# Kernel tuning notes

Hardware: AMD Instinct MI355X
Metric: run time of the kernel (lower is better)

## Reference

```python
import jax, jax.numpy as jnp
import numpy as np


def setup_inputs() -> dict:
    key = jax.random.key(0)
    k1, k2, k3, k4 = jax.random.split(key, 4)
    B, M, S, Q = 128, 200, 20, 20
    H, V, D = 3, 50000, 128  # max_hops, num_vocab, embedding_dim
    story = jax.random.randint(k1, (B, M, S), 0, V)
    query = jax.random.randint(k2, (B, Q), 0, V)
    # (max_hops+1) embedding tables, init normal(0, 0.1) as in torch code
    E = jax.random.normal(k3, (H + 1, V, D), dtype=jnp.float32) * 0.1
    # (max_hops+1) temporal encodings [max_story_size, D], normal(0, 0.1)
    T = jax.random.normal(k4, (H + 1, M, D), dtype=jnp.float32) * 0.1
    return {"story": story, "query": query, "E": E, "T": T}


def reference(story, query, E, T):
    max_hops = E.shape[0] - 1
    # u1 = sum over query tokens of B-embedding (hop-0 table)
    u = jnp.sum(E[0][query], axis=1)  # [B, D]
    for hop in range(max_hops):
        # memory: A-embed story, sum over words, add temporal encoding
        m = jnp.sum(E[hop][story], axis=2) + T[hop]        # [B, M, D]
        # attention over memories (legacy F.softmax on 2D -> dim=1)
        uTm = jnp.einsum('bmd,bd->bm', m, u)               # [B, M]
        proba = jax.nn.softmax(uTm, axis=1)
        # output memory representation
        c = jnp.sum(E[hop + 1][story], axis=2) + T[hop + 1]  # [B, M, D]
        o = jnp.einsum('bm,bmd->bd', proba, c)             # [B, D]
        u = u + o
    ahat = u @ E[-1].T  # [B, V]
    return ahat, jax.nn.softmax(ahat, axis=1)
```

## Files before the change

### kernel.cpp

```cpp
#include <hip/hip_runtime.h>
#include <float.h>


constexpr int Bn = 128;
constexpr int Mn = 200;
constexpr int Sn = 20;
constexpr int Qn = 20;
constexpr int Hn = 3;
constexpr int Vn = 50000;
constexpr int Dn = 128;
constexpr int CH = 100;

constexpr int GTILE = 128;
constexpr int NT    = (Vn + GTILE - 1) / GTILE;
constexpr int SMCHK = 10;

constexpr int TSTR = 130;

constexpr size_t MSUM_ELEMS = (size_t)(Hn + 1) * Bn * Mn * Dn;
constexpr size_t SMWS_ELEMS = (size_t)NT * Bn * 2;

typedef float f32x4 __attribute__((ext_vector_type(4)));

__global__ __launch_bounds__(256)
void msum_kernel(const int* __restrict__ story, const float* __restrict__ E,
                 const float* __restrict__ T, float* __restrict__ msum) {
    int slot = threadIdx.x >> 5;
    int l    = threadIdx.x & 31;
    int row  = blockIdx.x * 8 + slot;
    int t    = row / (Bn * Mn);
    int rem  = row - t * (Bn * Mn);
    int b    = rem / Mn;
    int m    = rem - b * Mn;

    const int* st = story + (b * Mn + m) * Sn;
    const float4* Tv = (const float4*)(T) + (size_t)(t * Mn + m) * 32;
    const float4* Et = (const float4*)(E) + (size_t)t * Vn * 32;

    int idx[Sn];
    #pragma unroll
    for (int s = 0; s < Sn; ++s) idx[s] = st[s];

    float4 acc = Tv[l];
    #pragma unroll
    for (int s = 0; s < Sn; ++s) {
        float4 e = Et[(size_t)idx[s] * 32 + l];
        acc.x += e.x; acc.y += e.y; acc.z += e.z; acc.w += e.w;
    }
    f32x4 av = {acc.x, acc.y, acc.z, acc.w};
    __builtin_nontemporal_store(av, (f32x4*)msum + (size_t)row * 32 + l);
}

__global__ __launch_bounds__(1024)
void hops_kernel(const int* __restrict__ query, const float* __restrict__ E,
                 const float* __restrict__ msum, float* __restrict__ ufin) {
    __shared__ __align__(16) float tileA[Mn * TSTR];
    __shared__ float u[Dn];
    __shared__ float sc[Mn];
    __shared__ float op[1024];
    __shared__ float red[16];
    __shared__ float bc[2];

    const int b    = blockIdx.x;
    const int tid  = threadIdx.x;
    const int wave = tid >> 6;
    const int lane = tid & 63;
    const int d    = tid & (Dn - 1);
    const int g    = tid >> 7;
    const int dq   = tid >> 8;
    const int mm   = tid & 255;

    {
        const float* src = msum + ((size_t)0 * Bn + b) * (size_t)(Mn * Dn);
        float2 vbuf[13];
        #pragma unroll
        for (int k = 0; k < 13; ++k) {
            int r = wave + 16 * k;
            if (r < Mn)
                vbuf[k] = *(const float2*)(src + (size_t)r * Dn + 2 * lane);
        }
        #pragma unroll
        for (int k = 0; k < 13; ++k) {
            int r = wave + 16 * k;
            if (r < Mn)
                *(float2*)(tileA + r * TSTR + 2 * lane) = vbuf[k];
        }
    }

    if (tid < Dn) {
        float acc = 0.f;
        const int* q = query + b * Qn;
        #pragma unroll
        for (int j = 0; j < Qn; ++j)
            acc += E[(size_t)q[j] * Dn + tid];
        u[tid] = acc;
    }
    __syncthreads();

    for (int hop = 0; hop < Hn; ++hop) {
        float2 vbuf[13];
        {
            const float* src = msum + ((size_t)(hop + 1) * Bn + b) * (size_t)(Mn * Dn);
            #pragma unroll
            for (int k = 0; k < 13; ++k) {
                int r = wave + 16 * k;
                if (r < Mn)
                    vbuf[k] = *(const float2*)(src + (size_t)r * Dn + 2 * lane);
            }
        }

        if (mm < Mn) {
            float p = 0.f;
            #pragma unroll
            for (int i = 0; i < 32; ++i)
                p += tileA[mm * TSTR + dq * 32 + i] * u[dq * 32 + i];
            op[dq * Mn + mm] = p;
        }
        __syncthreads();

        #pragma unroll
        for (int k = 0; k < 13; ++k) {
            int r = wave + 16 * k;
            if (r < Mn)
                *(float2*)(tileA + r * TSTR + 2 * lane) = vbuf[k];
        }

        float v = -FLT_MAX;
        if (tid < Mn)
            v = op[tid] + op[Mn + tid] + op[2 * Mn + tid] + op[3 * Mn + tid];
        float mx = v;
        #pragma unroll
        for (int off = 32; off; off >>= 1) mx = fmaxf(mx, __shfl_down(mx, off, 64));
        if (lane == 0) red[wave] = mx;
        __syncthreads();
        if (tid == 0) {
            float m0 = red[0];
            #pragma unroll
            for (int i = 1; i < 16; ++i) m0 = fmaxf(m0, red[i]);
            bc[0] = m0;
        }
        __syncthreads();
        float rmax = bc[0];
        float e = (tid < Mn) ? __expf(v - rmax) : 0.f;
        float sm = e;
        #pragma unroll
        for (int off = 32; off; off >>= 1) sm += __shfl_down(sm, off, 64);
        if (lane == 0) red[wave] = sm;
        __syncthreads();
        if (tid == 0) {
            float s = 0.f;
            #pragma unroll
            for (int i = 0; i < 16; ++i) s += red[i];
            bc[1] = s;
        }
        __syncthreads();
        float inv = 1.f / bc[1];
        if (tid < Mn) sc[tid] = e * inv;
        __syncthreads();

        float acc = 0.f;
        #pragma unroll
        for (int k = 0; k < 25; ++k) {
            int m = g + 8 * k;
            acc += sc[m] * tileA[m * TSTR + d];
        }
        op[g * Dn + d] = acc;
        __syncthreads();
        if (tid < Dn) {
            float s = 0.f;
            #pragma unroll
            for (int i = 0; i < 8; ++i) s += op[i * Dn + tid];
            u[tid] += s;
        }
        __syncthreads();
    }
    if (tid < Dn) ufin[b * Dn + tid] = u[tid];
}

__global__ __launch_bounds__(1024)
void hops_fused_kernel(const int* __restrict__ story, const int* __restrict__ query,
                       const float* __restrict__ E, const float* __restrict__ T,
                       float* __restrict__ ufin) {
    __shared__ __align__(16) float tile[CH * Dn];
    __shared__ float u[Dn];
    __shared__ float sc[Mn];
    __shared__ float op[8 * Dn];
    __shared__ float red[16];
    __shared__ float bc[2];

    const int b    = blockIdx.x;
    const int tid  = threadIdx.x;
    const int wave = tid >> 6;
    const int lane = tid & 63;
    const int d    = tid & (Dn - 1);
    const int g    = tid >> 7;
    const int slot = tid >> 5;
    const int l    = tid & 31;
    const int* st  = story + b * (Mn * Sn);

    if (tid < Dn) {
        float acc = 0.f;
        const int* q = query + b * Qn;
        #pragma unroll
        for (int j = 0; j < Qn; ++j)
            acc += E[(size_t)q[j] * Dn + tid];
        u[tid] = acc;
    }

    auto build = [&](int t, int base) {
        const float4* Et = (const float4*)(E) + (size_t)t * Vn * 32;
        const float4* Tt = (const float4*)(T) + (size_t)t * Mn * 32;
        for (int m = base + slot; m < base + CH; m += 32) {
            const int* sm = st + m * Sn;
            float4 acc = Tt[(size_t)m * 32 + l];
            #pragma unroll
            for (int s = 0; s < Sn; ++s) {
                float4 e = Et[(size_t)sm[s] * 32 + l];
                acc.x += e.x; acc.y += e.y; acc.z += e.z; acc.w += e.w;
            }
            ((float4*)tile)[(m - base) * 32 + l] = acc;
        }
    };
    auto scores = [&](int base) {
        for (int m = base + wave; m < base + CH; m += 16) {
            float p = tile[(m - base) * Dn + lane]      * u[lane]
                    + tile[(m - base) * Dn + lane + 64] * u[lane + 64];
            #pragma unroll
            for (int off = 32; off; off >>= 1) p += __shfl_down(p, off, 64);
            if (lane == 0) sc[m] = p;
        }
    };

    for (int hop = 0; hop < Hn; ++hop) {
        if (hop == 0) {
            build(0, 0);  __syncthreads(); scores(0);  __syncthreads();
            build(0, CH); __syncthreads(); scores(CH); __syncthreads();
        } else {
            scores(CH); __syncthreads();
            build(hop, 0); __syncthreads(); scores(0); __syncthreads();
        }

        float v = (tid < Mn) ? sc[tid] : -FLT_MAX;
        float mx = v;
        #pragma unroll
        for (int off = 32; off; off >>= 1) mx = fmaxf(mx, __shfl_down(mx, off, 64));
        if (lane == 0) red[wave] = mx;
        __syncthreads();
        if (tid == 0) {
            float m0 = red[0];
            #pragma unroll
            for (int i = 1; i < 16; ++i) m0 = fmaxf(m0, red[i]);
            bc[0] = m0;
        }
        __syncthreads();
        float rmax = bc[0];
        float e = (tid < Mn) ? __expf(v - rmax) : 0.f;
        float sm = e;
        #pragma unroll
        for (int off = 32; off; off >>= 1) sm += __shfl_down(sm, off, 64);
        if (lane == 0) red[wave] = sm;
        __syncthreads();
        if (tid == 0) {
            float s = 0.f;
            #pragma unroll
            for (int i = 0; i < 16; ++i) s += red[i];
            bc[1] = s;
        }
        __syncthreads();
        float inv = 1.f / bc[1];
        if (tid < Mn) sc[tid] = e * inv;

        float oacc = 0.f;
        build(hop + 1, 0);
        __syncthreads();
        for (int m = g; m < CH; m += 8)
            oacc += sc[m] * tile[m * Dn + d];
        __syncthreads();
        build(hop + 1, CH);
        __syncthreads();
        for (int m = CH + g; m < 2 * CH; m += 8)
            oacc += sc[m] * tile[(m - CH) * Dn + d];
        op[g * Dn + d] = oacc;
        __syncthreads();
        if (tid < Dn) {
            float s = 0.f;
            #pragma unroll
            for (int i = 0; i < 8; ++i) s += op[i * Dn + tid];
            u[tid] += s;
        }
        __syncthreads();
    }

    if (tid < Dn) ufin[b * Dn + tid] = u[tid];
}

constexpr int KC   = 32;
constexpr int LSTR = 140;
__device__ __forceinline__ int ldsCol(int c) { return c + 4 * (c >> 5); }

__global__ __launch_bounds__(256)
void ahat_gemm_kernel(const float* __restrict__ E, const float* __restrict__ ufin,
                      float* __restrict__ out, float* __restrict__ ws2) {
    __shared__ __align__(16) float uA[KC * LSTR];
    __shared__ __align__(16) float eB[KC * LSTR];
    const float* E3 = E + (size_t)Hn * Vn * Dn;

    const int tid   = threadIdx.x;
    const int tr    = tid & 15;
    const int tc    = tid >> 4;
    const int vbase = blockIdx.x * GTILE;

    const int f4 = tid & 7;
    const int rr = tid >> 3;

    float acc[8][8];
    #pragma unroll
    for (int i = 0; i < 8; ++i)
        #pragma unroll
        for (int j = 0; j < 8; ++j) acc[i][j] = 0.f;

    for (int kb = 0; kb < Dn; kb += KC) {
        #pragma unroll
        for (int i = 0; i < 4; ++i) {
            int r   = rr + 32 * i;
            int col = ldsCol(r);
            float4 uv = *(const float4*)(ufin + (size_t)r * Dn + kb + f4 * 4);
            uA[(f4 * 4 + 0) * LSTR + col] = uv.x;
            uA[(f4 * 4 + 1) * LSTR + col] = uv.y;
            uA[(f4 * 4 + 2) * LSTR + col] = uv.z;
            uA[(f4 * 4 + 3) * LSTR + col] = uv.w;
        }
        #pragma unroll
        for (int i = 0; i < 4; ++i) {
            int r  = rr + 32 * i;
            int vg = vbase + r; if (vg > Vn - 1) vg = Vn - 1;
            int col = ldsCol(r);
            float4 ev = *(const float4*)(E3 + (size_t)vg * Dn + kb + f4 * 4);
            eB[(f4 * 4 + 0) * LSTR + col] = ev.x;
            eB[(f4 * 4 + 1) * LSTR + col] = ev.y;
            eB[(f4 * 4 + 2) * LSTR + col] = ev.z;
            eB[(f4 * 4 + 3) * LSTR + col] = ev.w;
        }
        __syncthreads();
        const int ca = ldsCol(tr * 8);
        const int cb = ldsCol(tc * 8);
        #pragma unroll 2
        for (int k = 0; k < KC; ++k) {
            float4 a0 = *(const float4*)&uA[k * LSTR + ca];
            float4 a1 = *(const float4*)&uA[k * LSTR + ca + 4];
            float4 b0 = *(const float4*)&eB[k * LSTR + cb];
            float4 b1 = *(const float4*)&eB[k * LSTR + cb + 4];
            float av[8] = {a0.x, a0.y, a0.z, a0.w, a1.x, a1.y, a1.z, a1.w};
            float bv[8] = {b0.x, b0.y, b0.z, b0.w, b1.x, b1.y, b1.z, b1.w};
            #pragma unroll
            for (int i = 0; i < 8; ++i)
                #pragma unroll
                for (int j = 0; j < 8; ++j)
                    acc[i][j] += av[i] * bv[j];
        }
        __syncthreads();
    }

    const int  v0    = vbase + tc * 8;
    const bool valid = v0 < Vn;
    if (valid) {
        #pragma unroll
        for (int i = 0; i < 8; ++i) {
            int bb = tr * 8 + i;
            *(float4*)(out + (size_t)bb * Vn + v0) =
                make_float4(acc[i][0], acc[i][1], acc[i][2], acc[i][3]);
            *(float4*)(out + (size_t)bb * Vn + v0 + 4) =
                make_float4(acc[i][4], acc[i][5], acc[i][6], acc[i][7]);
        }
    }

    if (ws2) {
        #pragma unroll
        for (int i = 0; i < 8; ++i) {
            float tm = -FLT_MAX, ts = 0.f;
            if (valid) {
                #pragma unroll
                for (int j = 0; j < 8; ++j) tm = fmaxf(tm, acc[i][j]);
                #pragma unroll
                for (int j = 0; j < 8; ++j) ts += __expf(acc[i][j] - tm);
            }
            uA[tc * 128 + tr * 8 + i] = tm;
            eB[tc * 128 + tr * 8 + i] = ts;
        }
        __syncthreads();
        if (tid < Bn) {
            float M = -FLT_MAX;
            #pragma unroll
            for (int t = 0; t < 16; ++t) M = fmaxf(M, uA[t * 128 + tid]);
            float S = 0.f;
            #pragma unroll
            for (int t = 0; t < 16; ++t)
                S += eB[t * 128 + tid] * __expf(uA[t * 128 + tid] - M);
            float2* w = (float2*)ws2;
            w[(size_t)blockIdx.x * Bn + tid] = make_float2(M, S);
        }
    }
}

__global__ __launch_bounds__(256)
void softmax_merge_kernel(const float* __restrict__ ahat, const float* __restrict__ ws2,
                          float* __restrict__ osm) {
    __shared__ float redm[4], reds[4];
    __shared__ float bcM, bcI;

    const int ck   = blockIdx.x;
    const int b    = blockIdx.y;
    const int tid  = threadIdx.x;
    const int wave = tid >> 6;
    const int lane = tid & 63;

    float m = -FLT_MAX, s = 0.f;
    const float2* w = (const float2*)ws2;
    for (int i = tid; i < NT; i += 256) {
        float2 p = w[(size_t)i * Bn + b];
        float nm = fmaxf(m, p.x);
        s = s * __expf(m - nm) + p.y * __expf(p.x - nm);
        m = nm;
    }
    #pragma unroll
    for (int off = 32; off; off >>= 1) {
        float mo = __shfl_down(m, off, 64);
        float so = __shfl_down(s, off, 64);
        float nm = fmaxf(m, mo);
        s = s * __expf(m - nm) + so * __expf(mo - nm);
        m = nm;
    }
    if (lane == 0) { redm[wave] = m; reds[wave] = s; }
    __syncthreads();
    if (tid == 0) {
        float M = redm[0];
        #pragma unroll
        for (int i = 1; i < 4; ++i) M = fmaxf(M, redm[i]);
        float S = 0.f;
        #pragma unroll
        for (int i = 0; i < 4; ++i) S += reds[i] * __expf(redm[i] - M);
        bcM = M; bcI = 1.f / S;
    }
    __syncthreads();
    const float M   = bcM;
    const float inv = bcI;

    constexpr int C4 = Vn / SMCHK / 4;
    const float4* row  = (const float4*)(ahat + (size_t)b * Vn) + (size_t)ck * C4;
    float4*       orow = (float4*)(osm + (size_t)b * Vn) + (size_t)ck * C4;
    for (int v = tid; v < C4; v += 256) {
        float4 x = row[v];
        orow[v] = make_float4(__expf(x.x - M) * inv, __expf(x.y - M) * inv,
                              __expf(x.z - M) * inv, __expf(x.w - M) * inv);
    }
}

__global__ __launch_bounds__(1024)
void softmax_kernel(const float* __restrict__ ahat, float* __restrict__ osm) {
    __shared__ float redm[16];
    __shared__ float reds[16];
    __shared__ float bc2[2];

    int b    = blockIdx.x;
    int tid  = threadIdx.x;
    int wave = tid >> 6;
    int lane = tid & 63;

    const float4* row  = (const float4*)(ahat + (size_t)b * Vn);
    float4*       orow = (float4*)(osm + (size_t)b * Vn);
    constexpr int N4 = Vn / 4;

    float m = -FLT_MAX, s = 0.f;
    for (int v = tid; v < N4; v += 1024) {
        float4 x = row[v];
        float cm = fmaxf(fmaxf(x.x, x.y), fmaxf(x.z, x.w));
        if (cm > m) { s *= __expf(m - cm); m = cm; }
        s += __expf(x.x - m) + __expf(x.y - m) + __expf(x.z - m) + __expf(x.w - m);
    }
    #pragma unroll
    for (int off = 32; off; off >>= 1) {
        float mo = __shfl_down(m, off, 64);
        float so = __shfl_down(s, off, 64);
        float nm = fmaxf(m, mo);
        s = s * __expf(m - nm) + so * __expf(mo - nm);
        m = nm;
    }
    if (lane == 0) { redm[wave] = m; reds[wave] = s; }
    __syncthreads();
    if (tid == 0) {
        float M = redm[0];
        #pragma unroll
        for (int i = 1; i < 16; ++i) M = fmaxf(M, redm[i]);
        float S = 0.f;
        #pragma unroll
        for (int i = 0; i < 16; ++i) S += reds[i] * __expf(redm[i] - M);
        bc2[0] = M; bc2[1] = 1.f / S;
    }
    __syncthreads();
    float rmax = bc2[0];
    float inv  = bc2[1];

    for (int v = tid; v < N4; v += 1024) {
        float4 x = row[v];
        orow[v] = make_float4(__expf(x.x - rmax) * inv, __expf(x.y - rmax) * inv,
                              __expf(x.z - rmax) * inv, __expf(x.w - rmax) * inv);
    }
}

extern "C" void kernel_launch(void* const* d_in, const int* in_sizes, int n_in,
                              void* d_out, int out_size, void* d_ws, size_t ws_size,
                              hipStream_t stream) {
    const int*   story = (const int*)d_in[0];
    const int*   query = (const int*)d_in[1];
    const float* E     = (const float*)d_in[2];
    const float* T     = (const float*)d_in[3];

    float* out  = (float*)d_out;
    float* ufin = out + (size_t)Bn * Vn;

    const bool haveMsum = ws_size >= MSUM_ELEMS * sizeof(float);
    const bool haveSm   = ws_size >= (MSUM_ELEMS + SMWS_ELEMS) * sizeof(float);
    float* msum = (float*)d_ws;
    float* ws2  = haveSm ? ((float*)d_ws + MSUM_ELEMS) : nullptr;

    if (haveMsum) {
        msum_kernel<<<(Hn + 1) * Bn * Mn / 8, 256, 0, stream>>>(story, E, T, msum);
        hops_kernel<<<Bn, 1024, 0, stream>>>(query, E, msum, ufin);
    } else {
        hops_fused_kernel<<<Bn, 1024, 0, stream>>>(story, query, E, T, ufin);
    }

    ahat_gemm_kernel<<<NT, 256, 0, stream>>>(E, ufin, out, ws2);

    if (ws2) {
        softmax_merge_kernel<<<dim3(SMCHK, Bn), 256, 0, stream>>>(
            out, ws2, out + (size_t)Bn * Vn);
    } else {
        softmax_kernel<<<Bn, 1024, 0, stream>>>(out, out + (size_t)Bn * Vn);
    }
}
```

Baseline: 329.3 us.

## Fuse the vocab softmax into the GEMM epilogue via a grid-wide last-block merge

The separate softmax merge kernel is removed. Each GEMM block publishes its per-row partial max and sum and increments an atomic counter. The last block to arrive merges all partials into a global max and inverse sum, then releases a flag. Every block spins on that flag and writes the softmax output directly from its register accumulators, so the logits are no longer re-read from global memory. The msum store also changes from a nontemporal store to a plain store. The spin barrier assumes all 391 blocks are co-resident and adds a grid-wide synchronisation point.

```diff
diff --git a/kernel.cpp b/kernel.cpp
--- a/kernel.cpp
+++ b/kernel.cpp
@@ -13,14 +13,15 @@
 
 constexpr int GTILE = 128;
 constexpr int NT    = (Vn + GTILE - 1) / GTILE;
-constexpr int SMCHK = 10;
 
 constexpr int TSTR = 130;
 
 constexpr size_t MSUM_ELEMS = (size_t)(Hn + 1) * Bn * Mn * Dn;
 constexpr size_t SMWS_ELEMS = (size_t)NT * Bn * 2;
-
-typedef float f32x4 __attribute__((ext_vector_type(4)));
+constexpr size_t SMWS_TOTAL = SMWS_ELEMS + 256 + 8;
+
+#define AT_LD(p)    __hip_atomic_load((p), __ATOMIC_RELAXED, __HIP_MEMORY_SCOPE_AGENT)
+#define AT_ST(p, v) __hip_atomic_store((p), (v), __ATOMIC_RELAXED, __HIP_MEMORY_SCOPE_AGENT)
 
 __global__ __launch_bounds__(256)
 void msum_kernel(const int* __restrict__ story, const float* __restrict__ E,
@@ -47,13 +48,13 @@
         float4 e = Et[(size_t)idx[s] * 32 + l];
         acc.x += e.x; acc.y += e.y; acc.z += e.z; acc.w += e.w;
     }
-    f32x4 av = {acc.x, acc.y, acc.z, acc.w};
-    __builtin_nontemporal_store(av, (f32x4*)msum + (size_t)row * 32 + l);
+    ((float4*)msum)[(size_t)row * 32 + l] = acc;
 }
 
 __global__ __launch_bounds__(1024)
 void hops_kernel(const int* __restrict__ query, const float* __restrict__ E,
-                 const float* __restrict__ msum, float* __restrict__ ufin) {
+                 const float* __restrict__ msum, float* __restrict__ ufin,
+                 unsigned int* __restrict__ ctl) {
     __shared__ __align__(16) float tileA[Mn * TSTR];
     __shared__ float u[Dn];
     __shared__ float sc[Mn];
@@ -69,6 +70,11 @@
     const int g    = tid >> 7;
     const int dq   = tid >> 8;
     const int mm   = tid & 255;
+
+    if (ctl && b == 0 && tid == 0) {
+        AT_ST(ctl + 0, 0u);
+        AT_ST(ctl + 1, 0u);
+    }
 
     {
         const float* src = msum + ((size_t)0 * Bn + b) * (size_t)(Mn * Dn);
@@ -300,9 +306,11 @@
 
 __global__ __launch_bounds__(256)
 void ahat_gemm_kernel(const float* __restrict__ E, const float* __restrict__ ufin,
-                      float* __restrict__ out, float* __restrict__ ws2) {
+                      float* __restrict__ out, float* __restrict__ ws2,
+                      float* __restrict__ osm) {
     __shared__ __align__(16) float uA[KC * LSTR];
     __shared__ __align__(16) float eB[KC * LSTR];
+    __shared__ unsigned int amLast;
     const float* E3 = E + (size_t)Hn * Vn * Dn;
 
     const int tid   = threadIdx.x;
@@ -374,53 +382,129 @@
         }
     }
 
-    if (ws2) {
+    if (!ws2) return;
+
+    float* gs = ws2 + SMWS_ELEMS;
+    unsigned int* ctl = (unsigned int*)(gs + 256);
+
+    #pragma unroll
+    for (int i = 0; i < 8; ++i) {
+        float tm = -FLT_MAX, ts = 0.f;
+        if (valid) {
+            #pragma unroll
+            for (int j = 0; j < 8; ++j) tm = fmaxf(tm, acc[i][j]);
+            #pragma unroll
+            for (int j = 0; j < 8; ++j) ts += __expf(acc[i][j] - tm);
+        }
+        uA[tc * 128 + tr * 8 + i] = tm;
+        eB[tc * 128 + tr * 8 + i] = ts;
+    }
+    __syncthreads();
+    if (tid < Bn) {
+        float M = -FLT_MAX;
+        #pragma unroll
+        for (int t = 0; t < 16; ++t) M = fmaxf(M, uA[t * 128 + tid]);
+        float S = 0.f;
+        #pragma unroll
+        for (int t = 0; t < 16; ++t)
+            S += eB[t * 128 + tid] * __expf(uA[t * 128 + tid] - M);
+        float* wp = ws2 + ((size_t)blockIdx.x * Bn + tid) * 2;
+        AT_ST(wp + 0, M);
+        AT_ST(wp + 1, S);
+    }
+    __syncthreads();
+
+    if (tid == 0) {
+        __threadfence();
+        amLast = (atomicAdd(ctl + 0, 1u) == (unsigned)NT - 1) ? 1u : 0u;
+    }
+    __syncthreads();
+
+    if (amLast) {
+        const int r = tid & 127, h = tid >> 7;
+        float M = -FLT_MAX, S = 0.f;
+        for (int i = h; i < NT; i += 8) {
+            float pm[4], ps[4]; int n = 0;
+            #pragma unroll
+            for (int k = 0; k < 4; ++k) {
+                int t = i + 2 * k;
+                if (t < NT) {
+                    pm[n] = AT_LD(ws2 + ((size_t)t * Bn + r) * 2 + 0);
+                    ps[n] = AT_LD(ws2 + ((size_t)t * Bn + r) * 2 + 1);
+                    ++n;
+                }
+            }
+            for (int k = 0; k < n; ++k) {
+                float nm = fmaxf(M, pm[k]);
+                S = S * __expf(M - nm) + ps[k] * __expf(pm[k] - nm);
+                M = nm;
+            }
+        }
+        uA[h * 128 + r] = M;
+        eB[h * 128 + r] = S;
+        __syncthreads();
+        if (tid < 128) {
+            float m0 = uA[tid], m1 = uA[128 + tid];
+            float s0 = eB[tid], s1 = eB[128 + tid];
+            float nm = fmaxf(m0, m1);
+            float St = s0 * __expf(m0 - nm) + s1 * __expf(m1 - nm);
+            AT_ST(gs + tid * 2 + 0, nm);
+            AT_ST(gs + tid * 2 + 1, 1.f / St);
+        }
+        __syncthreads();
+        if (tid == 0) {
+            __threadfence();
+            __hip_atomic_store(ctl + 1, 1u, __ATOMIC_RELEASE, __HIP_MEMORY_SCOPE_AGENT);
+        }
+    }
+
+    if (tid == 0) {
+        long it = 0;
+        while (__hip_atomic_load(ctl + 1, __ATOMIC_ACQUIRE, __HIP_MEMORY_SCOPE_AGENT) == 0u
+               && it < 100000000L) {
+            ++it;
+            __builtin_amdgcn_s_sleep(8);
+        }
+    }
+    __syncthreads();
+
+    if (valid) {
         #pragma unroll
         for (int i = 0; i < 8; ++i) {
-            float tm = -FLT_MAX, ts = 0.f;
-            if (valid) {
-                #pragma unroll
-                for (int j = 0; j < 8; ++j) tm = fmaxf(tm, acc[i][j]);
-                #pragma unroll
-                for (int j = 0; j < 8; ++j) ts += __expf(acc[i][j] - tm);
-            }
-            uA[tc * 128 + tr * 8 + i] = tm;
-            eB[tc * 128 + tr * 8 + i] = ts;
-        }
-        __syncthreads();
-        if (tid < Bn) {
-            float M = -FLT_MAX;
-            #pragma unroll
-            for (int t = 0; t < 16; ++t) M = fmaxf(M, uA[t * 128 + tid]);
-            float S = 0.f;
-            #pragma unroll
-            for (int t = 0; t < 16; ++t)
-                S += eB[t * 128 + tid] * __expf(uA[t * 128 + tid] - M);
-            float2* w = (float2*)ws2;
-            w[(size_t)blockIdx.x * Bn + tid] = make_float2(M, S);
+            int bb = tr * 8 + i;
+            float M = AT_LD(gs + bb * 2 + 0);
+            float I = AT_LD(gs + bb * 2 + 1);
+            *(float4*)(osm + (size_t)bb * Vn + v0) =
+                make_float4(__expf(acc[i][0] - M) * I, __expf(acc[i][1] - M) * I,
+                            __expf(acc[i][2] - M) * I, __expf(acc[i][3] - M) * I);
+            *(float4*)(osm + (size_t)bb * Vn + v0 + 4) =
+                make_float4(__expf(acc[i][4] - M) * I, __expf(acc[i][5] - M) * I,
+                            __expf(acc[i][6] - M) * I, __expf(acc[i][7] - M) * I);
         }
     }
 }
 
-__global__ __launch_bounds__(256)
-void softmax_merge_kernel(const float* __restrict__ ahat, const float* __restrict__ ws2,
-                          float* __restrict__ osm) {
-    __shared__ float redm[4], reds[4];
-    __shared__ float bcM, bcI;
-
-    const int ck   = blockIdx.x;
-    const int b    = blockIdx.y;
-    const int tid  = threadIdx.x;
-    const int wave = tid >> 6;
-    const int lane = tid & 63;
+__global__ __launch_bounds__(1024)
+void softmax_kernel(const float* __restrict__ ahat, float* __restrict__ osm) {
+    __shared__ float redm[16];
+    __shared__ float reds[16];
+    __shared__ float bc2[2];
+
+    int b    = blockIdx.x;
+    int tid  = threadIdx.x;
+    int wave = tid >> 6;
+    int lane = tid & 63;
+
+    const float4* row  = (const float4*)(ahat + (size_t)b * Vn);
+    float4*       orow = (float4*)(osm + (size_t)b * Vn);
+    constexpr int N4 = Vn / 4;
 
     float m = -FLT_MAX, s = 0.f;
-    const float2* w = (const float2*)ws2;
-    for (int i = tid; i < NT; i += 256) {
-        float2 p = w[(size_t)i * Bn + b];
-        float nm = fmaxf(m, p.x);
-        s = s * __expf(m - nm) + p.y * __expf(p.x - nm);
-        m = nm;
+    for (int v = tid; v < N4; v += 1024) {
+        float4 x = row[v];
+        float cm = fmaxf(fmaxf(x.x, x.y), fmaxf(x.z, x.w));
+        if (cm > m) { s *= __expf(m - cm); m = cm; }
+        s += __expf(x.x - m) + __expf(x.y - m) + __expf(x.z - m) + __expf(x.w - m);
     }
     #pragma unroll
     for (int off = 32; off; off >>= 1) {
@@ -435,61 +519,6 @@
     if (tid == 0) {
         float M = redm[0];
         #pragma unroll
-        for (int i = 1; i < 4; ++i) M = fmaxf(M, redm[i]);
-        float S = 0.f;
-        #pragma unroll
-        for (int i = 0; i < 4; ++i) S += reds[i] * __expf(redm[i] - M);
-        bcM = M; bcI = 1.f / S;
-    }
-    __syncthreads();
-    const float M   = bcM;
-    const float inv = bcI;
-
-    constexpr int C4 = Vn / SMCHK / 4;
-    const float4* row  = (const float4*)(ahat + (size_t)b * Vn) + (size_t)ck * C4;
-    float4*       orow = (float4*)(osm + (size_t)b * Vn) + (size_t)ck * C4;
-    for (int v = tid; v < C4; v += 256) {
-        float4 x = row[v];
-        orow[v] = make_float4(__expf(x.x - M) * inv, __expf(x.y - M) * inv,
-                              __expf(x.z - M) * inv, __expf(x.w - M) * inv);
-    }
-}
-
-__global__ __launch_bounds__(1024)
-void softmax_kernel(const float* __restrict__ ahat, float* __restrict__ osm) {
-    __shared__ float redm[16];
-    __shared__ float reds[16];
-    __shared__ float bc2[2];
-
-    int b    = blockIdx.x;
-    int tid  = threadIdx.x;
-    int wave = tid >> 6;
-    int lane = tid & 63;
-
-    const float4* row  = (const float4*)(ahat + (size_t)b * Vn);
-    float4*       orow = (float4*)(osm + (size_t)b * Vn);
-    constexpr int N4 = Vn / 4;
-
-    float m = -FLT_MAX, s = 0.f;
-    for (int v = tid; v < N4; v += 1024) {
-        float4 x = row[v];
-        float cm = fmaxf(fmaxf(x.x, x.y), fmaxf(x.z, x.w));
-        if (cm > m) { s *= __expf(m - cm); m = cm; }
-        s += __expf(x.x - m) + __expf(x.y - m) + __expf(x.z - m) + __expf(x.w - m);
-    }
-    #pragma unroll
-    for (int off = 32; off; off >>= 1) {
-        float mo = __shfl_down(m, off, 64);
-        float so = __shfl_down(s, off, 64);
-        float nm = fmaxf(m, mo);
-        s = s * __expf(m - nm) + so * __expf(mo - nm);
-        m = nm;
-    }
-    if (lane == 0) { redm[wave] = m; reds[wave] = s; }
-    __syncthreads();
-    if (tid == 0) {
-        float M = redm[0];
-        #pragma unroll
         for (int i = 1; i < 16; ++i) M = fmaxf(M, redm[i]);
         float S = 0.f;
         #pragma unroll
@@ -516,26 +545,25 @@
     const float* T     = (const float*)d_in[3];
 
     float* out  = (float*)d_out;
-    float* ufin = out + (size_t)Bn * Vn;
+    float* osm  = out + (size_t)Bn * Vn;
+    float* ufin = osm;
 
     const bool haveMsum = ws_size >= MSUM_ELEMS * sizeof(float);
-    const bool haveSm   = ws_size >= (MSUM_ELEMS + SMWS_ELEMS) * sizeof(float);
+    const bool haveSm   = ws_size >= (MSUM_ELEMS + SMWS_TOTAL) * sizeof(float);
     float* msum = (float*)d_ws;
     float* ws2  = haveSm ? ((float*)d_ws + MSUM_ELEMS) : nullptr;
+    unsigned int* ctl = haveSm ? (unsigned int*)(ws2 + SMWS_ELEMS + 256) : nullptr;
 
     if (haveMsum) {
         msum_kernel<<<(Hn + 1) * Bn * Mn / 8, 256, 0, stream>>>(story, E, T, msum);
-        hops_kernel<<<Bn, 1024, 0, stream>>>(query, E, msum, ufin);
+        hops_kernel<<<Bn, 1024, 0, stream>>>(query, E, msum, ufin, ctl);
     } else {
         hops_fused_kernel<<<Bn, 1024, 0, stream>>>(story, query, E, T, ufin);
     }
 
-    ahat_gemm_kernel<<<NT, 256, 0, stream>>>(E, ufin, out, ws2);
-
-    if (ws2) {
-        softmax_merge_kernel<<<dim3(SMCHK, Bn), 256, 0, stream>>>(
-            out, ws2, out + (size_t)Bn * Vn);
-    } else {
-        softmax_kernel<<<Bn, 1024, 0, stream>>>(out, out + (size_t)Bn * Vn);
+    ahat_gemm_kernel<<<NT, 256, 0, stream>>>(E, ufin, out, ws2, osm);
+
+    if (!ws2) {
+        softmax_kernel<<<Bn, 1024, 0, stream>>>(out, osm);
     }
 }
```

New measurement: 570.5 us. 73.2% more time.
